# Kernel tuning notes

Hardware: AMD Instinct MI355X
Metric: run time of the kernel (lower is better)

## Reference

```python
import jax, jax.numpy as jnp
import numpy as np

B, T = 4, 512
IN, OUT, D, HID = 80, 4096, 512, 1024
E, NB, LPB = 4, 2, 4
NL = NB * LPB
H, M = 8, 64
LB, LA, SL, SR = 4, 1, 2, 1


def setup_inputs():
    key = jax.random.key(0)
    it = iter(jax.random.split(key, 40))
    def nrm(shape, s=0.02):
        return jax.random.normal(next(it), shape, jnp.float32) * s
    return {
        'x': jax.random.normal(next(it), (B, T, IN), jnp.float32),
        'seq_len': jax.random.randint(next(it), (B,), T // 2, T + 1),
        'emb_w1': nrm((IN, HID)), 'emb_b1': jnp.zeros((HID,), jnp.float32),
        'emb_w2': nrm((HID, D)), 'emb_wo': nrm((D, OUT)),
        'f0_w1': nrm((E, IN, HID)), 'f0_b1': jnp.zeros((E, HID), jnp.float32),
        'f0_w2': nrm((E, HID, D)), 'f0_router': nrm((D, E)),
        'f0_fb': nrm((LB, D), 0.1), 'f0_fa': nrm((LA, D), 0.1),
        'f_w1': nrm((NL - 1, E, D, HID)), 'f_b1': jnp.zeros((NL - 1, E, HID), jnp.float32),
        'f_w2': nrm((NL - 1, E, HID, D)), 'f_router': nrm((NL - 1, D, E)),
        'f_fb': nrm((NL - 1, LB, D), 0.1), 'f_fa': nrm((NL - 1, LA, D), 0.1),
        'attn_wq': nrm((NB, D, D)), 'attn_wk': nrm((NB, D, D)),
        'attn_wv': nrm((NB, D, D)), 'attn_wo': nrm((NB, D, D)),
        'attn_mk': nrm((NB, M, D)), 'attn_mv': nrm((NB, M, D)),
        'ln_g': jnp.ones((NB, D), jnp.float32), 'ln_b': jnp.zeros((NB, D), jnp.float32),
        'out_w': nrm((D, OUT)), 'out_b': jnp.zeros((OUT,), jnp.float32),
    }


def _fsmn_memory(p, fb, fa):
    # m[t] = p[t] + sum_k fb[k]*p[t-(k+1)*SL] + sum_j fa[j]*p[t+(j+1)*SR]  (depthwise)
    m = p
    for k in range(fb.shape[0]):
        off = (k + 1) * SL
        past = jnp.pad(p, ((0, 0), (off, 0), (0, 0)))[:, :p.shape[1]]
        m = m + past * fb[k]
    for j in range(fa.shape[0]):
        off = (j + 1) * SR
        fut = jnp.pad(p, ((0, 0), (0, off), (0, 0)))[:, off:]
        m = m + fut * fa[j]
    return m


def _pe(dtype):
    pos = jnp.arange(T, dtype=jnp.float32)[:, None]
    div = jnp.exp(jnp.arange(0, D, 2, dtype=jnp.float32) * (-np.log(10000.0) / D))
    pe = jnp.zeros((T, D), jnp.float32)
    pe = pe.at[:, 0::2].set(jnp.sin(pos * div)).at[:, 1::2].set(jnp.cos(pos * div))
    return pe.astype(dtype)


def _layernorm(x, g, b):
    mu = jnp.mean(x, -1, keepdims=True)
    var = jnp.var(x, -1, keepdims=True)
    return (x - mu) * jax.lax.rsqrt(var + 1e-5) * g + b


def reference(x, seq_len, emb_w1, emb_b1, emb_w2, emb_wo,
              f0_w1, f0_b1, f0_w2, f0_router, f0_fb, f0_fa,
              f_w1, f_b1, f_w2, f_router, f_fb, f_fa,
              attn_wq, attn_wk, attn_wv, attn_wo, attn_mk, attn_mv,
              ln_g, ln_b, out_w, out_b):
    tok_mask = jnp.arange(T)[None, :] < seq_len[:, None]  # [B,T] valid frames

    # embed sub-network (router features; detached as in Net.forward)
    embed = jax.nn.relu(x @ emb_w1 + emb_b1) @ emb_w2      # [B,T,D]
    embed_out = embed @ emb_wo                             # [B,T,OUT]
    embed_r = jax.lax.stop_gradient(embed)

    def moe_fsmn(xi, w1, b1, w2, router, fb, fa, skip):
        gates = jax.nn.softmax(embed_r @ router, axis=-1)  # [B,T,E]
        g = jnp.max(gates, axis=-1)
        disp = jax.nn.one_hot(jnp.argmax(gates, -1), E, dtype=xi.dtype) * g[..., None]
        h = jax.nn.relu(jnp.einsum('bti,eih->beth', xi, w1) + b1[None, :, None, :])
        p = jnp.einsum('beth,ehd->betd', h, w2)            # low-rank expert proj
        p = jnp.einsum('bte,betd->btd', disp, p)           # top-1 combine
        m = _fsmn_memory(p, fb, fa)
        if skip:
            m = m + xi
        imp = jnp.sum(gates * tok_mask[..., None].astype(gates.dtype), axis=(0, 1))
        aux = jnp.var(imp) / (jnp.mean(imp) ** 2 + 1e-9)   # importance cv^2
        return m, aux

    def attention(xi, wq, wk, wv, wo, mk, mv, g, b):
        dh = D // H
        q = (xi @ wq).reshape(B, T, H, dh)
        k = jnp.concatenate([xi @ wk, jnp.broadcast_to(mk, (B, M, D))], 1).reshape(B, T + M, H, dh)
        v = jnp.concatenate([xi @ wv, jnp.broadcast_to(mv, (B, M, D))], 1).reshape(B, T + M, H, dh)
        scores = jnp.einsum('bthd,bshd->bhts', q, k) / np.sqrt(dh).astype(np.float32)
        key_ok = jnp.concatenate([tok_mask, jnp.ones((B, M), bool)], 1)  # memory keys never masked
        scores = jnp.where(key_ok[:, None, None, :], scores, jnp.float32(-1e9))
        a = jax.nn.softmax(scores, -1)
        o = jnp.einsum('bhts,bshd->bthd', a, v).reshape(B, T, D) @ wo
        return _layernorm(xi + o, g, b)

    auxes = []
    cur = x
    li = 0
    for blk in range(NB):
        for _ in range(LPB):
            if li == 0:
                cur, aux = moe_fsmn(cur, f0_w1, f0_b1, f0_w2, f0_router, f0_fb, f0_fa, False)
            else:
                j = li - 1
                cur, aux = moe_fsmn(cur, f_w1[j], f_b1[j], f_w2[j], f_router[j], f_fb[j], f_fa[j], True)
            auxes.append(aux)
            li += 1
        if blk == 0:
            cur = cur + _pe(cur.dtype)[None]
        cur = attention(cur, attn_wq[blk], attn_wk[blk], attn_wv[blk], attn_wo[blk],
                        attn_mk[blk], attn_mv[blk], ln_g[blk], ln_b[blk])
    out = cur @ out_w + out_b
    return out, embed_out, jnp.stack(auxes).sum()
```

## Files before the change

### kernel.cpp

```cpp
#include <hip/hip_runtime.h>
#include <hip/hip_bf16.h>


typedef __bf16 bf16x8 __attribute__((ext_vector_type(8)));
typedef float f32x4 __attribute__((ext_vector_type(4)));

#define B_ 4
#define T_ 512
#define IN_ 80
#define OUT_ 4096
#define D_ 512
#define HID_ 1024
#define E_ 4
#define H_ 8
#define DH_ 64
#define M_ 64
#define BT_ (B_ * T_)
#define TKV_ (T_ + M_)
#define RBLK_ (BT_ / 4)

__device__ __forceinline__ unsigned pk2(float a, float b) {
    unsigned short ua = __builtin_bit_cast(unsigned short, (__bf16)a);
    unsigned short ub = __builtin_bit_cast(unsigned short, (__bf16)b);
    return (unsigned)ua | ((unsigned)ub << 16);
}
__device__ __forceinline__ unsigned pkh2(__bf16 a, __bf16 b) {
    unsigned short ua = __builtin_bit_cast(unsigned short, a);
    unsigned short ub = __builtin_bit_cast(unsigned short, b);
    return (unsigned)ua | ((unsigned)ub << 16);
}

__global__ __launch_bounds__(256) void gemm80_k(
    const float* __restrict__ A,
    const float* __restrict__ Bw,
    const float* __restrict__ bias,
    float* __restrict__ C)
{
    __shared__ float As[80][68];
    __shared__ float Bs[80][68];
    int m0 = blockIdx.y * 64, n0 = blockIdx.x * 64;
    int tid = threadIdx.x;
#pragma unroll
    for (int i = 0; i < 5; i++) {
        int idx = tid + 256 * i;
        int m = idx / 20, c = idx % 20;
        float4 f = *(const float4*)&A[(size_t)(m0 + m) * 80 + c * 4];
        As[c * 4 + 0][m] = f.x; As[c * 4 + 1][m] = f.y;
        As[c * 4 + 2][m] = f.z; As[c * 4 + 3][m] = f.w;
    }
#pragma unroll
    for (int i = 0; i < 5; i++) {
        int idx = tid + 256 * i;
        int k = idx / 16, c = idx % 16;
        float4 f = *(const float4*)&Bw[(size_t)k * 1024 + n0 + c * 4];
        *(float4*)&Bs[k][c * 4] = f;
    }
    __syncthreads();
    int tx = tid & 15, ty = tid >> 4;
    float acc[4][4];
#pragma unroll
    for (int j = 0; j < 4; j++)
#pragma unroll
        for (int i = 0; i < 4; i++) acc[j][i] = 0.f;
#pragma unroll 8
    for (int k = 0; k < 80; k++) {
        float4 a = *(const float4*)&As[k][ty * 4];
        float4 b = *(const float4*)&Bs[k][tx * 4];
        float av[4] = {a.x, a.y, a.z, a.w};
        float bv[4] = {b.x, b.y, b.z, b.w};
#pragma unroll
        for (int j = 0; j < 4; j++)
#pragma unroll
            for (int i = 0; i < 4; i++) acc[j][i] += av[j] * bv[i];
    }
#pragma unroll
    for (int j = 0; j < 4; j++) {
        size_t row = (size_t)(m0 + ty * 4 + j);
        float4 o;
        o.x = fmaxf(acc[j][0] + bias[n0 + tx * 4 + 0], 0.f);
        o.y = fmaxf(acc[j][1] + bias[n0 + tx * 4 + 1], 0.f);
        o.z = fmaxf(acc[j][2] + bias[n0 + tx * 4 + 2], 0.f);
        o.w = fmaxf(acc[j][3] + bias[n0 + tx * 4 + 3], 0.f);
        *(float4*)&C[row * 1024 + n0 + tx * 4] = o;
    }
}

__global__ void wr2_k(const float* __restrict__ w2,
                      const float* __restrict__ r0,
                      const float* __restrict__ rl,
                      float* __restrict__ R2)
{
    int wv = threadIdx.x >> 6, lane = threadIdx.x & 63;
    int h = blockIdx.x * 4 + wv;
    const float* wrow = w2 + (size_t)h * 512;
    float w[8];
#pragma unroll
    for (int i = 0; i < 8; i++) w[i] = wrow[lane + 64 * i];
    for (int l = 0; l < 8; l++) {
        const float* rp = (l == 0) ? r0 : rl + (size_t)(l - 1) * 2048;
        double a0 = 0, a1 = 0, a2 = 0, a3 = 0;
#pragma unroll
        for (int i = 0; i < 8; i++) {
            int d = lane + 64 * i;
            float4 r = *(const float4*)&rp[d * 4];
            a0 += (double)w[i] * (double)r.x;
            a1 += (double)w[i] * (double)r.y;
            a2 += (double)w[i] * (double)r.z;
            a3 += (double)w[i] * (double)r.w;
        }
        for (int off = 32; off; off >>= 1) {
            a0 += __shfl_xor(a0, off); a1 += __shfl_xor(a1, off);
            a2 += __shfl_xor(a2, off); a3 += __shfl_xor(a3, off);
        }
        if (lane == 0) {
            float4 o = make_float4((float)a0, (float)a1, (float)a2, (float)a3);
            *(float4*)&R2[((size_t)l * 1024 + h) * 4] = o;
        }
    }
}

__global__ __launch_bounds__(256) void routerall_k(
    const float* __restrict__ h,
    const float* __restrict__ R2,
    const int* __restrict__ seq_len,
    int* __restrict__ eid,
    float* __restrict__ gatev,
    float* __restrict__ impPart)
{
    __shared__ float impLoc[4][32];
    int wv = threadIdx.x >> 6, lane = threadIdx.x & 63;
    int tok = blockIdx.x * 4 + wv;
    const float* hr = h + (size_t)tok * 1024;
    float acc[8][4];
#pragma unroll
    for (int l = 0; l < 8; l++)
#pragma unroll
        for (int e = 0; e < 4; e++) acc[l][e] = 0.f;
    for (int i = 0; i < 16; i++) {
        int d = lane + 64 * i;
        float hv = hr[d];
#pragma unroll
        for (int l = 0; l < 8; l++) {
            float4 r = *(const float4*)&R2[((size_t)l * 1024 + d) * 4];
            acc[l][0] += hv * r.x; acc[l][1] += hv * r.y;
            acc[l][2] += hv * r.z; acc[l][3] += hv * r.w;
        }
    }
    for (int off = 32; off; off >>= 1) {
#pragma unroll
        for (int l = 0; l < 8; l++)
#pragma unroll
            for (int e = 0; e < 4; e++) acc[l][e] += __shfl_xor(acc[l][e], off);
    }
    if (lane == 0) {
        int b = tok >> 9, t = tok & 511;
        bool valid = t < seq_len[b];
        for (int l = 0; l < 8; l++) {
            float lg[4] = {acc[l][0], acc[l][1], acc[l][2], acc[l][3]};
            float mx = fmaxf(fmaxf(lg[0], lg[1]), fmaxf(lg[2], lg[3]));
            float g[4], s = 0.f;
            for (int e = 0; e < 4; e++) { g[e] = expf(lg[e] - mx); s += g[e]; }
            float inv = 1.f / s;
            int am = 0; float bv = g[0];
            for (int e = 1; e < 4; e++) if (g[e] > bv) { bv = g[e]; am = e; }
            eid[l * BT_ + tok] = am;
            gatev[l * BT_ + tok] = bv * inv;
            for (int e = 0; e < 4; e++)
                impLoc[wv][l * 4 + e] = valid ? g[e] * inv : 0.f;
        }
    }
    __syncthreads();
    int tid = threadIdx.x;
    if (tid < 32) {
        float s = impLoc[0][tid] + impLoc[1][tid] + impLoc[2][tid] + impLoc[3][tid];
        impPart[(size_t)blockIdx.x * 32 + tid] = s;
    }
}

__global__ void cvtw_k(const float* __restrict__ src, __bf16* __restrict__ dst,
                       int nsh, int kpsh, int Ksrc)
{
    int idx = blockIdx.x * 256 + threadIdx.x;
    int cprsh = nsh - 3;
    int row = idx >> cprsh;
    int chunk = idx & ((1 << cprsh) - 1);
    int e = row >> kpsh, k = row & ((1 << kpsh) - 1);
    int n = chunk * 8;
    uint4 pk;
    if (k < Ksrc) {
        const float* sp = src + (((size_t)e * Ksrc + k) << nsh) + n;
        float4 f0 = *(const float4*)sp;
        float4 f1 = *(const float4*)(sp + 4);
        pk = make_uint4(pk2(f0.x, f0.y), pk2(f0.z, f0.w),
                        pk2(f1.x, f1.y), pk2(f1.z, f1.w));
    } else pk = make_uint4(0, 0, 0, 0);
    *(uint4*)&dst[(((size_t)row) << nsh) + n] = pk;
}

__global__ void gathera_k(const float* __restrict__ src, int lda,
                          const int* __restrict__ sorted,
                          __bf16* __restrict__ dst, int kpsh, int Ksrc)
{
    int idx = blockIdx.x * 256 + threadIdx.x;
    int cprsh = kpsh - 3;
    int row = idx >> cprsh;
    int chunk = idx & ((1 << cprsh) - 1);
    int k0 = chunk * 8;
    uint4 pk;
    if (k0 < Ksrc) {
        const float* sp = src + (size_t)sorted[row] * lda + k0;
        float4 f0 = *(const float4*)sp;
        float4 f1 = *(const float4*)(sp + 4);
        pk = make_uint4(pk2(f0.x, f0.y), pk2(f0.z, f0.w),
                        pk2(f1.x, f1.y), pk2(f1.z, f1.w));
    } else pk = make_uint4(0, 0, 0, 0);
    *(uint4*)&dst[((size_t)row << kpsh) + k0] = pk;
}

template<bool W1OUT>
__global__ __launch_bounds__(256) void egemm_k(
    const __bf16* __restrict__ Ag, const __bf16* __restrict__ Bh,
    const float* __restrict__ bias,
    __bf16* __restrict__ Cb, float* __restrict__ Cf,
    int N, int Kpad,
    const int* __restrict__ seg, const int* __restrict__ sorted,
    const float* __restrict__ scale)
{
    __shared__ __align__(16) __bf16 As[2][128 * 64];
    __shared__ __align__(16) __bf16 Bs[2][64 * 64];

    int e = blockIdx.z;
    int row0 = seg[e], cnt = seg[e + 1] - row0;
    int m0 = blockIdx.y * 128;
    if (m0 >= cnt) return;
    int n0 = blockIdx.x * 64;
    const __bf16* Bp = Bh + (size_t)e * Kpad * N;

    int tid = threadIdx.x;
    int arow = tid >> 1, ahalf = tid & 1;
    const __bf16* aptr = Ag + (size_t)(row0 + m0 + arow) * Kpad + ahalf * 32;
    int asb = arow * 64;
    int ac0 = ahalf * 4;
    int arx = arow & 7;
    int bn = tid & 63, bkc = tid >> 6;
    const __bf16* bptr = Bp + n0 + bn;
    int bsb = bn * 64;
    int brx = bn & 7;

    int lane = tid & 63, wid = tid >> 6;
    int wm = wid & 1, wn = wid >> 1;
    int l15 = lane & 15, quad = lane >> 4;

    int aoff[4][2], boff[2][2];
#pragma unroll
    for (int mt = 0; mt < 4; mt++) {
        int m = wm * 64 + mt * 16 + l15;
#pragma unroll
        for (int s = 0; s < 2; s++)
            aoff[mt][s] = m * 64 + (((s * 4 + quad) ^ (m & 7)) * 8);
    }
#pragma unroll
    for (int nt = 0; nt < 2; nt++) {
        int n = wn * 32 + nt * 16 + l15;
#pragma unroll
        for (int s = 0; s < 2; s++)
            boff[nt][s] = n * 64 + (((s * 4 + quad) ^ (n & 7)) * 8);
    }

    f32x4 acc[4][2];
#pragma unroll
    for (int mt = 0; mt < 4; mt++)
#pragma unroll
        for (int nt = 0; nt < 2; nt++)
#pragma unroll
            for (int r = 0; r < 4; r++) acc[mt][nt][r] = 0.f;

    uint4 rA[4]; unsigned rB[8];
    auto stage = [&](int k0) {
#pragma unroll
        for (int j = 0; j < 4; j++) rA[j] = *(const uint4*)(aptr + k0 + j * 8);
#pragma unroll
        for (int c = 0; c < 2; c++) {
            int kk = k0 + (bkc * 2 + c) * 8;
#pragma unroll
            for (int i = 0; i < 4; i++)
                rB[c * 4 + i] = pkh2(bptr[(size_t)(kk + 2 * i) * N],
                                     bptr[(size_t)(kk + 2 * i + 1) * N]);
        }
    };
    auto commit = [&](int buf) {
#pragma unroll
        for (int j = 0; j < 4; j++)
            *(uint4*)&As[buf][asb + (((ac0 + j) ^ arx) * 8)] = rA[j];
#pragma unroll
        for (int c = 0; c < 2; c++)
            *(uint4*)&Bs[buf][bsb + (((bkc * 2 + c) ^ brx) * 8)] =
                make_uint4(rB[c * 4 + 0], rB[c * 4 + 1], rB[c * 4 + 2], rB[c * 4 + 3]);
    };

    stage(0); commit(0); __syncthreads();
    int nt_ = Kpad >> 6;
    for (int t = 0; t < nt_; t++) {
        int buf = t & 1;
        if (t + 1 < nt_) stage((t + 1) << 6);
        bf16x8 af[4][2], bfr[2][2];
#pragma unroll
        for (int mt = 0; mt < 4; mt++)
#pragma unroll
            for (int s = 0; s < 2; s++)
                af[mt][s] = *(const bf16x8*)&As[buf][aoff[mt][s]];
#pragma unroll
        for (int ntx = 0; ntx < 2; ntx++)
#pragma unroll
            for (int s = 0; s < 2; s++)
                bfr[ntx][s] = *(const bf16x8*)&Bs[buf][boff[ntx][s]];
#pragma unroll
        for (int mt = 0; mt < 4; mt++)
#pragma unroll
            for (int ntx = 0; ntx < 2; ntx++)
#pragma unroll
                for (int s = 0; s < 2; s++)
                    acc[mt][ntx] = __builtin_amdgcn_mfma_f32_16x16x32_bf16(
                        af[mt][s], bfr[ntx][s], acc[mt][ntx], 0, 0, 0);
        if (t + 1 < nt_) commit(buf ^ 1);
        __syncthreads();
    }

#pragma unroll
    for (int mt = 0; mt < 4; mt++) {
#pragma unroll
        for (int r = 0; r < 4; r++) {
            int m = m0 + wm * 64 + mt * 16 + quad * 4 + r;
            if (m >= cnt) continue;
            if (W1OUT) {
                size_t ci = (size_t)(row0 + m);
#pragma unroll
                for (int ntx = 0; ntx < 2; ntx++) {
                    int col = n0 + wn * 32 + ntx * 16 + l15;
                    float v = acc[mt][ntx][r] + bias[e * N + col];
                    Cb[ci * N + col] = (__bf16)fmaxf(v, 0.f);
                }
            } else {
                int tok = sorted[row0 + m];
                float sc = scale[tok];
#pragma unroll
                for (int ntx = 0; ntx < 2; ntx++) {
                    int col = n0 + wn * 32 + ntx * 16 + l15;
                    Cf[(size_t)tok * N + col] = acc[mt][ntx][r] * sc;
                }
            }
        }
    }
}

#define MBM 128
#define MBN 64
#define MBK 32
#define LDAS 40

template<bool RELU, bool BIAS>
__global__ __launch_bounds__(256) void mgemm_k(
    const float* __restrict__ A, int lda,
    const float* __restrict__ Bw, const float* __restrict__ bias,
    float* __restrict__ C, int ldc, int M, int N, int K, int remM)
{
    __shared__ __align__(16) __bf16 As[MBM * LDAS];
    __shared__ __align__(16) __bf16 Bs[MBN * LDAS];

    int m0 = blockIdx.y * MBM;
    int n0 = blockIdx.x * MBN;

    int tid = threadIdx.x;
    int arow = tid >> 1, ahalf = tid & 1;
    const float* aptr = A + (size_t)(m0 + arow) * lda + ahalf * 16;
    int asw = (arow >> 3) & 3;
    int bn = tid & 63, bkc = tid >> 6;
    int bcs = bkc ^ ((bn >> 3) & 3);

    int lane = tid & 63, wid = tid >> 6;
    int wm = wid & 1, wn = wid >> 1;
    int l15 = lane & 15, quad = lane >> 4;

    int aoff[4], boff[2];
#pragma unroll
    for (int mt = 0; mt < 4; mt++) {
        int m = wm * 64 + mt * 16 + l15;
        aoff[mt] = m * LDAS + (quad ^ ((m >> 3) & 3)) * 8;
    }
#pragma unroll
    for (int nt = 0; nt < 2; nt++) {
        int n = wn * 32 + nt * 16 + l15;
        boff[nt] = n * LDAS + (quad ^ ((n >> 3) & 3)) * 8;
    }

    f32x4 acc[4][2];
#pragma unroll
    for (int mt = 0; mt < 4; mt++)
#pragma unroll
        for (int nt = 0; nt < 2; nt++)
#pragma unroll
            for (int r = 0; r < 4; r++) acc[mt][nt][r] = 0.f;

    for (int k0 = 0; k0 < K; k0 += MBK) {
#pragma unroll
        for (int cc = 0; cc < 2; cc++) {
            float4 f0 = *(const float4*)(aptr + k0 + cc * 8);
            float4 f1 = *(const float4*)(aptr + k0 + cc * 8 + 4);
            uint4 pk = make_uint4(pk2(f0.x, f0.y), pk2(f0.z, f0.w),
                                  pk2(f1.x, f1.y), pk2(f1.z, f1.w));
            int cs = (ahalf * 2 + cc) ^ asw;
            *(uint4*)&As[arow * LDAS + cs * 8] = pk;
        }
        {
            float f[8];
            int kk = k0 + bkc * 8;
#pragma unroll
            for (int i = 0; i < 8; i++)
                f[i] = Bw[(size_t)(kk + i) * N + n0 + bn];
            uint4 pk = make_uint4(pk2(f[0], f[1]), pk2(f[2], f[3]),
                                  pk2(f[4], f[5]), pk2(f[6], f[7]));
            *(uint4*)&Bs[bn * LDAS + bcs * 8] = pk;
        }
        __syncthreads();
        bf16x8 af[4], bfm[2];
#pragma unroll
        for (int mt = 0; mt < 4; mt++) af[mt] = *(const bf16x8*)&As[aoff[mt]];
#pragma unroll
        for (int nt = 0; nt < 2; nt++) bfm[nt] = *(const bf16x8*)&Bs[boff[nt]];
#pragma unroll
        for (int mt = 0; mt < 4; mt++)
#pragma unroll
            for (int nt = 0; nt < 2; nt++)
                acc[mt][nt] = __builtin_amdgcn_mfma_f32_16x16x32_bf16(
                    af[mt], bfm[nt], acc[mt][nt], 0, 0, 0);
        __syncthreads();
    }

#pragma unroll
    for (int mt = 0; mt < 4; mt++) {
#pragma unroll
        for (int r = 0; r < 4; r++) {
            int mi = wm * 64 + mt * 16 + quad * 4 + r;
            int m = m0 + mi;
            size_t crow = (size_t)m;
            if (remM) crow = (size_t)m + (size_t)(m >> 9) * remM;
#pragma unroll
            for (int nt = 0; nt < 2; nt++) {
                int col = n0 + wn * 32 + nt * 16 + l15;
                float v = acc[mt][nt][r];
                if (BIAS) v += bias[col];
                if (RELU) v = fmaxf(v, 0.f);
                C[crow * (size_t)ldc + col] = v;
            }
        }
    }
}

__global__ __launch_bounds__(256) void qkv_k(
    const float* __restrict__ A,
    const float* __restrict__ wq, const float* __restrict__ wk,
    const float* __restrict__ wv,
    float* __restrict__ qo, float* __restrict__ ko, float* __restrict__ vo)
{
    __shared__ __align__(16) __bf16 As[MBM * LDAS];
    __shared__ __align__(16) __bf16 Bs[MBN * LDAS];

    int n0g = blockIdx.x * MBN;
    int which = n0g >> 9;
    int n0 = n0g & 511;
    const float* Bp = (which == 0) ? wq : (which == 1) ? wk : wv;
    float* Cp = (which == 0) ? qo : (which == 1) ? ko : vo;
    int m0 = blockIdx.y * MBM;

    int tid = threadIdx.x;
    int arow = tid >> 1, ahalf = tid & 1;
    const float* aptr = A + (size_t)(m0 + arow) * D_ + ahalf * 16;
    int asw = (arow >> 3) & 3;
    int bn = tid & 63, bkc = tid >> 6;
    int bcs = bkc ^ ((bn >> 3) & 3);

    int lane = tid & 63, wid = tid >> 6;
    int wm = wid & 1, wn = wid >> 1;
    int l15 = lane & 15, quad = lane >> 4;

    int aoff[4], boff[2];
#pragma unroll
    for (int mt = 0; mt < 4; mt++) {
        int m = wm * 64 + mt * 16 + l15;
        aoff[mt] = m * LDAS + (quad ^ ((m >> 3) & 3)) * 8;
    }
#pragma unroll
    for (int nt = 0; nt < 2; nt++) {
        int n = wn * 32 + nt * 16 + l15;
        boff[nt] = n * LDAS + (quad ^ ((n >> 3) & 3)) * 8;
    }

    f32x4 acc[4][2];
#pragma unroll
    for (int mt = 0; mt < 4; mt++)
#pragma unroll
        for (int nt = 0; nt < 2; nt++)
#pragma unroll
            for (int r = 0; r < 4; r++) acc[mt][nt][r] = 0.f;

    for (int k0 = 0; k0 < D_; k0 += MBK) {
#pragma unroll
        for (int cc = 0; cc < 2; cc++) {
            float4 f0 = *(const float4*)(aptr + k0 + cc * 8);
            float4 f1 = *(const float4*)(aptr + k0 + cc * 8 + 4);
            uint4 pk = make_uint4(pk2(f0.x, f0.y), pk2(f0.z, f0.w),
                                  pk2(f1.x, f1.y), pk2(f1.z, f1.w));
            int cs = (ahalf * 2 + cc) ^ asw;
            *(uint4*)&As[arow * LDAS + cs * 8] = pk;
        }
        {
            float f[8];
            int kk = k0 + bkc * 8;
#pragma unroll
            for (int i = 0; i < 8; i++)
                f[i] = Bp[(size_t)(kk + i) * D_ + n0 + bn];
            uint4 pk = make_uint4(pk2(f[0], f[1]), pk2(f[2], f[3]),
                                  pk2(f[4], f[5]), pk2(f[6], f[7]));
            *(uint4*)&Bs[bn * LDAS + bcs * 8] = pk;
        }
        __syncthreads();
        bf16x8 af[4], bfm[2];
#pragma unroll
        for (int mt = 0; mt < 4; mt++) af[mt] = *(const bf16x8*)&As[aoff[mt]];
#pragma unroll
        for (int nt = 0; nt < 2; nt++) bfm[nt] = *(const bf16x8*)&Bs[boff[nt]];
#pragma unroll
        for (int mt = 0; mt < 4; mt++)
#pragma unroll
            for (int nt = 0; nt < 2; nt++)
                acc[mt][nt] = __builtin_amdgcn_mfma_f32_16x16x32_bf16(
                    af[mt], bfm[nt], acc[mt][nt], 0, 0, 0);
        __syncthreads();
    }

#pragma unroll
    for (int mt = 0; mt < 4; mt++) {
#pragma unroll
        for (int r = 0; r < 4; r++) {
            int mi = wm * 64 + mt * 16 + quad * 4 + r;
            int m = m0 + mi;
            size_t crow = which ? (size_t)(m + (m >> 9) * M_) : (size_t)m;
#pragma unroll
            for (int nt = 0; nt < 2; nt++) {
                int col = n0 + wn * 32 + nt * 16 + l15;
                Cp[crow * (size_t)D_ + col] = acc[mt][nt][r];
            }
        }
    }
}

__global__ void bucketall_k(const int* __restrict__ eidA, int* __restrict__ sortedA,
                            int* __restrict__ segA)
{
    __shared__ int cnt[E_]; __shared__ int cur[E_];
    int l = blockIdx.x;
    const int* eid = eidA + l * BT_;
    int* sorted = sortedA + l * BT_;
    int* seg = segA + l * 8;
    int tid = threadIdx.x;
    if (tid < E_) cnt[tid] = 0;
    __syncthreads();
    for (int t = tid; t < BT_; t += 256) atomicAdd(&cnt[eid[t]], 1);
    __syncthreads();
    if (tid == 0) {
        int o = 0;
        for (int e = 0; e < E_; e++) { seg[e] = o; cur[e] = o; o += cnt[e]; }
        seg[E_] = o;
    }
    __syncthreads();
    for (int t = tid; t < BT_; t += 256) {
        int pos = atomicAdd(&cur[eid[t]], 1);
        sorted[pos] = t;
    }
}

__global__ void fsmn_k(const float* __restrict__ p, const float* __restrict__ fb,
                       const float* __restrict__ fa, float* __restrict__ cur, int skip)
{
    int idx = blockIdx.x * 256 + threadIdx.x;
    int d = idx & 511;
    int t = (idx >> 9) & 511;
    float m = p[idx];
#pragma unroll
    for (int k = 0; k < 4; k++) {
        int tt = t - 2 * (k + 1);
        if (tt >= 0) m += fb[k * D_ + d] * p[idx - D_ * 2 * (k + 1)];
    }
    if (t + 1 < T_) m += fa[d] * p[idx + D_];
    if (skip) m += cur[idx];
    cur[idx] = m;
}

__global__ void addpe_k(float* __restrict__ cur) {
    int idx = blockIdx.x * 256 + threadIdx.x;
    int d = idx & 511, t = (idx >> 9) & 511;
    float div = expf((float)(d & ~1) * (-9.210340371976184f / (float)D_));
    float ang = (float)t * div;
    cur[idx] += (d & 1) ? cosf(ang) : sinf(ang);
}

__global__ void fillmem_k(const float* __restrict__ mk, const float* __restrict__ mv,
                          float* __restrict__ kbuf, float* __restrict__ vbuf)
{
    int idx = blockIdx.x * 256 + threadIdx.x;
    int d = idx & 511, m = (idx >> 9) & 63, b = idx >> 15;
    size_t row = (size_t)b * TKV_ + T_ + m;
    kbuf[row * D_ + d] = mk[m * D_ + d];
    vbuf[row * D_ + d] = mv[m * D_ + d];
}

#define QR 16
__global__ __launch_bounds__(256) void attn_k(
    const float* __restrict__ q, const float* __restrict__ kbuf,
    const float* __restrict__ vbuf, const int* __restrict__ seq_len,
    float* __restrict__ attno)
{
    __shared__ float kv[64 * 69];
    __shared__ float qs[QR][64];
    __shared__ float sc[QR][TKV_];
    int b = blockIdx.z, h = blockIdx.y, t0 = blockIdx.x * QR;
    int tid = threadIdx.x, w = tid >> 6, lane = tid & 63;
    int r0 = w * 4;
#pragma unroll
    for (int i = 0; i < 4; i++) {
        int idx = tid + 256 * i;
        int r = idx >> 6, d = idx & 63;
        qs[r][d] = q[((size_t)(b * T_) + t0 + r) * D_ + h * DH_ + d] * 0.125f;
    }
    int sl = seq_len[b];
    for (int s0 = 0; s0 < TKV_; s0 += 64) {
        __syncthreads();
#pragma unroll
        for (int i = 0; i < 16; i++) {
            int idx = tid + 256 * i;
            int key = idx >> 6, d = idx & 63;
            kv[d * 69 + key] = kbuf[((size_t)b * TKV_ + s0 + key) * D_ + h * DH_ + d];
        }
        __syncthreads();
        float a0 = 0, a1 = 0, a2 = 0, a3 = 0;
#pragma unroll 4
        for (int d = 0; d < 64; d++) {
            float kvv = kv[d * 69 + lane];
            a0 += qs[r0 + 0][d] * kvv;
            a1 += qs[r0 + 1][d] * kvv;
            a2 += qs[r0 + 2][d] * kvv;
            a3 += qs[r0 + 3][d] * kvv;
        }
        int sa = s0 + lane;
        bool ok = (sa >= T_ || sa < sl);
        sc[r0 + 0][sa] = ok ? a0 : -1e9f;
        sc[r0 + 1][sa] = ok ? a1 : -1e9f;
        sc[r0 + 2][sa] = ok ? a2 : -1e9f;
        sc[r0 + 3][sa] = ok ? a3 : -1e9f;
    }
    float inv[4];
#pragma unroll
    for (int r = 0; r < 4; r++) {
        float mx = -1e30f;
        for (int s = lane; s < TKV_; s += 64) mx = fmaxf(mx, sc[r0 + r][s]);
        for (int off = 32; off; off >>= 1) mx = fmaxf(mx, __shfl_xor(mx, off));
        float sum = 0.f;
        for (int s = lane; s < TKV_; s += 64) {
            float e2 = expf(sc[r0 + r][s] - mx); sc[r0 + r][s] = e2; sum += e2;
        }
        for (int off = 32; off; off >>= 1) sum += __shfl_xor(sum, off);
        inv[r] = 1.f / sum;
    }
    float o0 = 0, o1 = 0, o2 = 0, o3 = 0;
    for (int s0 = 0; s0 < TKV_; s0 += 64) {
        __syncthreads();
#pragma unroll
        for (int i = 0; i < 16; i++) {
            int idx = tid + 256 * i;
            int key = idx >> 6, d = idx & 63;
            kv[key * 69 + d] = vbuf[((size_t)b * TKV_ + s0 + key) * D_ + h * DH_ + d];
        }
        __syncthreads();
#pragma unroll 4
        for (int j = 0; j < 64; j++) {
            float vv = kv[j * 69 + lane];
            o0 += sc[r0 + 0][s0 + j] * vv;
            o1 += sc[r0 + 1][s0 + j] * vv;
            o2 += sc[r0 + 2][s0 + j] * vv;
            o3 += sc[r0 + 3][s0 + j] * vv;
        }
    }
    size_t base = ((size_t)(b * T_) + t0 + r0) * D_ + h * DH_ + lane;
    attno[base + 0 * D_] = o0 * inv[0];
    attno[base + 1 * D_] = o1 * inv[1];
    attno[base + 2 * D_] = o2 * inv[2];
    attno[base + 3 * D_] = o3 * inv[3];
}

__global__ void ln_k(const float* __restrict__ o, const float* __restrict__ g,
                     const float* __restrict__ bb, float* __restrict__ cur)
{
    int w = threadIdx.x >> 6, lane = threadIdx.x & 63;
    size_t row = (size_t)(blockIdx.x * 4 + w);
    float v[8]; float s = 0.f;
#pragma unroll
    for (int i = 0; i < 8; i++) {
        int d = lane + 64 * i;
        v[i] = cur[row * D_ + d] + o[row * D_ + d];
        s += v[i];
    }
    for (int off = 32; off; off >>= 1) s += __shfl_xor(s, off);
    float mu = s * (1.f / D_);
    float vs = 0.f;
#pragma unroll
    for (int i = 0; i < 8; i++) { float dd = v[i] - mu; vs += dd * dd; }
    for (int off = 32; off; off >>= 1) vs += __shfl_xor(vs, off);
    float rstd = rsqrtf(vs * (1.f / D_) + 1e-5f);
#pragma unroll
    for (int i = 0; i < 8; i++) {
        int d = lane + 64 * i;
        cur[row * D_ + d] = (v[i] - mu) * rstd * g[d] + bb[d];
    }
}

__global__ __launch_bounds__(256) void aux_k(const float* __restrict__ impPart,
                                             float* __restrict__ outp)
{
    __shared__ float red[8][32];
    __shared__ float imp[32];
    int tid = threadIdx.x;
    int c = tid & 31, p = tid >> 5;
    float s = 0.f;
    for (int b = p; b < RBLK_; b += 8) s += impPart[(size_t)b * 32 + c];
    red[p][c] = s;
    __syncthreads();
    if (tid < 32) {
        float t = 0.f;
#pragma unroll
        for (int i = 0; i < 8; i++) t += red[i][tid];
        imp[tid] = t;
    }
    __syncthreads();
    if (tid == 0) {
        float total = 0.f;
        for (int l = 0; l < 8; l++) {
            const float* ip = imp + l * 4;
            float m = (ip[0] + ip[1] + ip[2] + ip[3]) * 0.25f;
            float var = 0.f;
            for (int e = 0; e < 4; e++) { float d = ip[e] - m; var += d * d; }
            var *= 0.25f;
            total += var / (m * m + 1e-9f);
        }
        *outp = total;
    }
}

extern "C" void kernel_launch(void* const* d_in, const int* in_sizes, int n_in,
                              void* d_out, int out_size, void* d_ws, size_t ws_size,
                              hipStream_t stream)
{
    (void)in_sizes; (void)n_in; (void)out_size; (void)ws_size;
    const float* x        = (const float*)d_in[0];
    const int*   seqlen   = (const int*)d_in[1];
    const float* emb_w1   = (const float*)d_in[2];
    const float* emb_b1   = (const float*)d_in[3];
    const float* emb_w2   = (const float*)d_in[4];
    const float* emb_wo   = (const float*)d_in[5];
    const float* f0_w1    = (const float*)d_in[6];
    const float* f0_b1    = (const float*)d_in[7];
    const float* f0_w2    = (const float*)d_in[8];
    const float* f0_router= (const float*)d_in[9];
    const float* f0_fb    = (const float*)d_in[10];
    const float* f0_fa    = (const float*)d_in[11];
    const float* f_w1     = (const float*)d_in[12];
    const float* f_b1     = (const float*)d_in[13];
    const float* f_w2     = (const float*)d_in[14];
    const float* f_router = (const float*)d_in[15];
    const float* f_fb     = (const float*)d_in[16];
    const float* f_fa     = (const float*)d_in[17];
    const float* attn_wq  = (const float*)d_in[18];
    const float* attn_wk  = (const float*)d_in[19];
    const float* attn_wv  = (const float*)d_in[20];
    const float* attn_wo  = (const float*)d_in[21];
    const float* attn_mk  = (const float*)d_in[22];
    const float* attn_mv  = (const float*)d_in[23];
    const float* ln_g     = (const float*)d_in[24];
    const float* ln_b     = (const float*)d_in[25];
    const float* out_w    = (const float*)d_in[26];
    const float* out_b    = (const float*)d_in[27];

    float* out0 = (float*)d_out;
    float* out1 = out0 + (size_t)BT_ * OUT_;
    float* out2 = out1 + (size_t)BT_ * OUT_;

    float* fws = (float*)d_ws;
    size_t o = 0;
    float* embedF = fws + o; o += (size_t)BT_ * D_;
    float* curB   = fws + o; o += (size_t)BT_ * D_;
    float* hbuf   = fws + o; o += (size_t)BT_ * HID_;
    float* pbuf   = fws + o; o += (size_t)BT_ * D_;
    float* kbuf   = fws + o; o += (size_t)B_ * TKV_ * D_;
    float* vbuf   = fws + o; o += (size_t)B_ * TKV_ * D_;
    float* gatev  = fws + o; o += (size_t)8 * BT_;
    float* impPart= fws + o; o += (size_t)RBLK_ * 32;
    float* R2     = fws + o; o += (size_t)8 * 1024 * 4;
    int* eid     = (int*)(fws + o); o += (size_t)8 * BT_;
    int* sortedA = (int*)(fws + o); o += (size_t)8 * BT_;
    int* segA    = (int*)(fws + o); o += 64;
    __bf16* Ag    = (__bf16*)hbuf;
    __bf16* hbufh = (__bf16*)(hbuf + (size_t)BT_ * D_ / 2);
    __bf16* w1h   = (__bf16*)kbuf;
    __bf16* w2h   = (__bf16*)vbuf;
    float* qbuf  = pbuf;
    float* attno = hbuf;
    float* tmpo  = hbuf + (size_t)BT_ * D_;

    gemm80_k<<<dim3(HID_ / 64, BT_ / 64, 1), 256, 0, stream>>>(x, emb_w1, emb_b1, hbuf);
    wr2_k<<<256, 256, 0, stream>>>(emb_w2, f0_router, f_router, R2);
    routerall_k<<<RBLK_, 256, 0, stream>>>(hbuf, R2, seqlen, eid, gatev, impPart);
    bucketall_k<<<8, 256, 0, stream>>>(eid, sortedA, segA);
    mgemm_k<false,false><<<dim3(D_/MBN, BT_/MBM, 1), 256, 0, stream>>>(
        hbuf, HID_, emb_w2, nullptr, embedF, D_, BT_, D_, HID_, 0);
    mgemm_k<false,false><<<dim3(OUT_/MBN, BT_/MBM, 1), 256, 0, stream>>>(
        embedF, D_, emb_wo, nullptr, out1, OUT_, BT_, OUT_, D_, 0);

    for (int l = 0; l < 8; l++) {
        const float* w1  = (l == 0) ? f0_w1 : f_w1 + (size_t)(l-1) * E_ * D_ * HID_;
        const float* b1p = (l == 0) ? f0_b1 : f_b1 + (size_t)(l-1) * E_ * HID_;
        const float* w2  = (l == 0) ? f0_w2 : f_w2 + (size_t)(l-1) * E_ * HID_ * D_;
        const float* fbp = (l == 0) ? f0_fb : f_fb + (size_t)(l-1) * 4 * D_;
        const float* fap = (l == 0) ? f0_fa : f_fa + (size_t)(l-1) * 1 * D_;
        const float* Ain = (l == 0) ? x : curB;
        int lda  = (l == 0) ? IN_ : D_;
        int Ks   = (l == 0) ? IN_ : D_;
        int Kp   = (l == 0) ? 128 : 512;
        int kpsh = (l == 0) ? 7 : 9;
        const int* seg = segA + l * 8;
        const int* sorted = sortedA + l * BT_;

        cvtw_k<<<E_ * Kp * HID_ / 8 / 256, 256, 0, stream>>>(w1, w1h, 10, kpsh, Ks);
        cvtw_k<<<E_ * HID_ * D_ / 8 / 256, 256, 0, stream>>>(w2, w2h, 9, 10, HID_);
        gathera_k<<<BT_ * Kp / 8 / 256, 256, 0, stream>>>(Ain, lda, sorted, Ag, kpsh, Ks);

        egemm_k<true><<<dim3(HID_/64, BT_/128, E_), 256, 0, stream>>>(
            Ag, w1h, b1p, hbufh, nullptr, HID_, Kp, seg, nullptr, nullptr);
        egemm_k<false><<<dim3(D_/64, BT_/128, E_), 256, 0, stream>>>(
            hbufh, w2h, nullptr, nullptr, pbuf, D_, HID_, seg, sorted, gatev + l * BT_);
        fsmn_k<<<BT_*D_/256, 256, 0, stream>>>(pbuf, fbp, fap, curB, (l > 0) ? 1 : 0);

        if (l == 3) addpe_k<<<BT_*D_/256, 256, 0, stream>>>(curB);

        if (l == 3 || l == 7) {
            int ab = (l == 3) ? 0 : 1;
            const float* wq = attn_wq + (size_t)ab * D_ * D_;
            const float* wk = attn_wk + (size_t)ab * D_ * D_;
            const float* wv = attn_wv + (size_t)ab * D_ * D_;
            const float* wo = attn_wo + (size_t)ab * D_ * D_;
            const float* mk = attn_mk + (size_t)ab * M_ * D_;
            const float* mv = attn_mv + (size_t)ab * M_ * D_;
            const float* g  = ln_g + (size_t)ab * D_;
            const float* bb = ln_b + (size_t)ab * D_;

            qkv_k<<<dim3(3 * D_ / MBN, BT_ / MBM, 1), 256, 0, stream>>>(
                curB, wq, wk, wv, qbuf, kbuf, vbuf);
            fillmem_k<<<B_*M_*D_/256, 256, 0, stream>>>(mk, mv, kbuf, vbuf);
            attn_k<<<dim3(T_/QR, H_, B_), 256, 0, stream>>>(qbuf, kbuf, vbuf, seqlen, attno);
            mgemm_k<false,false><<<dim3(D_/MBN, BT_/MBM, 1), 256, 0, stream>>>(
                attno, D_, wo, nullptr, tmpo, D_, BT_, D_, D_, 0);
            ln_k<<<BT_/4, 256, 0, stream>>>(tmpo, g, bb, curB);
        }
    }

    mgemm_k<false,true><<<dim3(OUT_/MBN, BT_/MBM, 1), 256, 0, stream>>>(
        curB, D_, out_w, out_b, out0, OUT_, BT_, OUT_, D_, 0);
    aux_k<<<1, 256, 0, stream>>>(impPart, out2);
}
```

Measured before the change: 1.423 ms.

## Double-buffer dense GEMMs with bf16 weights and skip masked attention key tiles

Replaces the generic dense GEMM with a double-buffered kernel using K-tiles of 64. Weights are converted to bf16 up front, so the B operand is read at half width and global loads overlap the MFMA work. The attention kernel now visits only key tiles up to the sequence length plus the memory tile, and vectorises its score and PV inner loops. It adds extra conversion launches per call and reuses scratch buffers for the bf16 weights, which risks aliasing if those buffers are still live.

```diff
diff --git a/kernel.cpp b/kernel.cpp
--- a/kernel.cpp
+++ b/kernel.cpp
@@ -353,26 +353,150 @@
     }
 }
 
+template<bool BIAS>
+__global__ __launch_bounds__(256) void dgemm_k(
+    const float* __restrict__ A,
+    const __bf16* __restrict__ Bh,
+    const float* __restrict__ bias,
+    float* __restrict__ C,
+    int N, int K)
+{
+    __shared__ __align__(16) __bf16 As[2][128 * 64];
+    __shared__ __align__(16) __bf16 Bs[2][64 * 64];
+
+    int m0 = blockIdx.y * 128, n0 = blockIdx.x * 64;
+    int tid = threadIdx.x;
+    int arow = tid >> 1, ahalf = tid & 1;
+    const float* aptr = A + (size_t)(m0 + arow) * K + ahalf * 32;
+    int asb = arow * 64, ac0 = ahalf * 4, arx = arow & 7;
+    int bn = tid & 63, bkc = tid >> 6;
+    const __bf16* bptr = Bh + n0 + bn;
+    int bsb = bn * 64, brx = bn & 7;
+
+    int lane = tid & 63, wid = tid >> 6;
+    int wm = wid & 1, wn = wid >> 1;
+    int l15 = lane & 15, quad = lane >> 4;
+
+    int aoff[4][2], boff[2][2];
+#pragma unroll
+    for (int mt = 0; mt < 4; mt++) {
+        int m = wm * 64 + mt * 16 + l15;
+#pragma unroll
+        for (int s = 0; s < 2; s++)
+            aoff[mt][s] = m * 64 + (((s * 4 + quad) ^ (m & 7)) * 8);
+    }
+#pragma unroll
+    for (int nt = 0; nt < 2; nt++) {
+        int n = wn * 32 + nt * 16 + l15;
+#pragma unroll
+        for (int s = 0; s < 2; s++)
+            boff[nt][s] = n * 64 + (((s * 4 + quad) ^ (n & 7)) * 8);
+    }
+
+    f32x4 acc[4][2];
+#pragma unroll
+    for (int mt = 0; mt < 4; mt++)
+#pragma unroll
+        for (int nt = 0; nt < 2; nt++)
+#pragma unroll
+            for (int r = 0; r < 4; r++) acc[mt][nt][r] = 0.f;
+
+    uint4 rA[4]; unsigned rB[8];
+    auto stage = [&](int k0) {
+#pragma unroll
+        for (int j = 0; j < 4; j++) {
+            float4 f0 = *(const float4*)(aptr + k0 + j * 8);
+            float4 f1 = *(const float4*)(aptr + k0 + j * 8 + 4);
+            rA[j] = make_uint4(pk2(f0.x, f0.y), pk2(f0.z, f0.w),
+                               pk2(f1.x, f1.y), pk2(f1.z, f1.w));
+        }
+#pragma unroll
+        for (int c = 0; c < 2; c++) {
+            int kk = k0 + (bkc * 2 + c) * 8;
+#pragma unroll
+            for (int i = 0; i < 4; i++)
+                rB[c * 4 + i] = pkh2(bptr[(size_t)(kk + 2 * i) * N],
+                                     bptr[(size_t)(kk + 2 * i + 1) * N]);
+        }
+    };
+    auto commit = [&](int buf) {
+#pragma unroll
+        for (int j = 0; j < 4; j++)
+            *(uint4*)&As[buf][asb + (((ac0 + j) ^ arx) * 8)] = rA[j];
+#pragma unroll
+        for (int c = 0; c < 2; c++)
+            *(uint4*)&Bs[buf][bsb + (((bkc * 2 + c) ^ brx) * 8)] =
+                make_uint4(rB[c * 4 + 0], rB[c * 4 + 1], rB[c * 4 + 2], rB[c * 4 + 3]);
+    };
+
+    stage(0); commit(0); __syncthreads();
+    int nt_ = K >> 6;
+    for (int t = 0; t < nt_; t++) {
+        int buf = t & 1;
+        if (t + 1 < nt_) stage((t + 1) << 6);
+        bf16x8 af[4][2], bfr[2][2];
+#pragma unroll
+        for (int mt = 0; mt < 4; mt++)
+#pragma unroll
+            for (int s = 0; s < 2; s++)
+                af[mt][s] = *(const bf16x8*)&As[buf][aoff[mt][s]];
+#pragma unroll
+        for (int ntx = 0; ntx < 2; ntx++)
+#pragma unroll
+            for (int s = 0; s < 2; s++)
+                bfr[ntx][s] = *(const bf16x8*)&Bs[buf][boff[ntx][s]];
+#pragma unroll
+        for (int mt = 0; mt < 4; mt++)
+#pragma unroll
+            for (int ntx = 0; ntx < 2; ntx++)
+#pragma unroll
+                for (int s = 0; s < 2; s++)
+                    acc[mt][ntx] = __builtin_amdgcn_mfma_f32_16x16x32_bf16(
+                        af[mt][s], bfr[ntx][s], acc[mt][ntx], 0, 0, 0);
+        if (t + 1 < nt_) commit(buf ^ 1);
+        __syncthreads();
+    }
+
+#pragma unroll
+    for (int mt = 0; mt < 4; mt++) {
+#pragma unroll
+        for (int r = 0; r < 4; r++) {
+            int m = m0 + wm * 64 + mt * 16 + quad * 4 + r;
+#pragma unroll
+            for (int ntx = 0; ntx < 2; ntx++) {
+                int col = n0 + wn * 32 + ntx * 16 + l15;
+                float v = acc[mt][ntx][r];
+                if (BIAS) v += bias[col];
+                C[(size_t)m * N + col] = v;
+            }
+        }
+    }
+}
+
 #define MBM 128
 #define MBN 64
 #define MBK 32
 #define LDAS 40
 
-template<bool RELU, bool BIAS>
-__global__ __launch_bounds__(256) void mgemm_k(
-    const float* __restrict__ A, int lda,
-    const float* __restrict__ Bw, const float* __restrict__ bias,
-    float* __restrict__ C, int ldc, int M, int N, int K, int remM)
+__global__ __launch_bounds__(256) void qkv_k(
+    const float* __restrict__ A,
+    const __bf16* __restrict__ wq, const __bf16* __restrict__ wk,
+    const __bf16* __restrict__ wv,
+    float* __restrict__ qo, float* __restrict__ ko, float* __restrict__ vo)
 {
     __shared__ __align__(16) __bf16 As[MBM * LDAS];
     __shared__ __align__(16) __bf16 Bs[MBN * LDAS];
 
+    int n0g = blockIdx.x * MBN;
+    int which = n0g >> 9;
+    int n0 = n0g & 511;
+    const __bf16* Bp = (which == 0) ? wq : (which == 1) ? wk : wv;
+    float* Cp = (which == 0) ? qo : (which == 1) ? ko : vo;
     int m0 = blockIdx.y * MBM;
-    int n0 = blockIdx.x * MBN;
 
     int tid = threadIdx.x;
     int arow = tid >> 1, ahalf = tid & 1;
-    const float* aptr = A + (size_t)(m0 + arow) * lda + ahalf * 16;
+    const float* aptr = A + (size_t)(m0 + arow) * D_ + ahalf * 16;
     int asw = (arow >> 3) & 3;
     int bn = tid & 63, bkc = tid >> 6;
     int bcs = bkc ^ ((bn >> 3) & 3);
@@ -401,7 +525,7 @@
 #pragma unroll
             for (int r = 0; r < 4; r++) acc[mt][nt][r] = 0.f;
 
-    for (int k0 = 0; k0 < K; k0 += MBK) {
+    for (int k0 = 0; k0 < D_; k0 += MBK) {
 #pragma unroll
         for (int cc = 0; cc < 2; cc++) {
             float4 f0 = *(const float4*)(aptr + k0 + cc * 8);
@@ -412,115 +536,13 @@
             *(uint4*)&As[arow * LDAS + cs * 8] = pk;
         }
         {
-            float f[8];
-            int kk = k0 + bkc * 8;
-#pragma unroll
-            for (int i = 0; i < 8; i++)
-                f[i] = Bw[(size_t)(kk + i) * N + n0 + bn];
-            uint4 pk = make_uint4(pk2(f[0], f[1]), pk2(f[2], f[3]),
-                                  pk2(f[4], f[5]), pk2(f[6], f[7]));
-            *(uint4*)&Bs[bn * LDAS + bcs * 8] = pk;
-        }
-        __syncthreads();
-        bf16x8 af[4], bfm[2];
-#pragma unroll
-        for (int mt = 0; mt < 4; mt++) af[mt] = *(const bf16x8*)&As[aoff[mt]];
-#pragma unroll
-        for (int nt = 0; nt < 2; nt++) bfm[nt] = *(const bf16x8*)&Bs[boff[nt]];
-#pragma unroll
-        for (int mt = 0; mt < 4; mt++)
-#pragma unroll
-            for (int nt = 0; nt < 2; nt++)
-                acc[mt][nt] = __builtin_amdgcn_mfma_f32_16x16x32_bf16(
-                    af[mt], bfm[nt], acc[mt][nt], 0, 0, 0);
-        __syncthreads();
-    }
-
-#pragma unroll
-    for (int mt = 0; mt < 4; mt++) {
-#pragma unroll
-        for (int r = 0; r < 4; r++) {
-            int mi = wm * 64 + mt * 16 + quad * 4 + r;
-            int m = m0 + mi;
-            size_t crow = (size_t)m;
-            if (remM) crow = (size_t)m + (size_t)(m >> 9) * remM;
-#pragma unroll
-            for (int nt = 0; nt < 2; nt++) {
-                int col = n0 + wn * 32 + nt * 16 + l15;
-                float v = acc[mt][nt][r];
-                if (BIAS) v += bias[col];
-                if (RELU) v = fmaxf(v, 0.f);
-                C[crow * (size_t)ldc + col] = v;
-            }
-        }
-    }
-}
-
-__global__ __launch_bounds__(256) void qkv_k(
-    const float* __restrict__ A,
-    const float* __restrict__ wq, const float* __restrict__ wk,
-    const float* __restrict__ wv,
-    float* __restrict__ qo, float* __restrict__ ko, float* __restrict__ vo)
-{
-    __shared__ __align__(16) __bf16 As[MBM * LDAS];
-    __shared__ __align__(16) __bf16 Bs[MBN * LDAS];
-
-    int n0g = blockIdx.x * MBN;
-    int which = n0g >> 9;
-    int n0 = n0g & 511;
-    const float* Bp = (which == 0) ? wq : (which == 1) ? wk : wv;
-    float* Cp = (which == 0) ? qo : (which == 1) ? ko : vo;
-    int m0 = blockIdx.y * MBM;
-
-    int tid = threadIdx.x;
-    int arow = tid >> 1, ahalf = tid & 1;
-    const float* aptr = A + (size_t)(m0 + arow) * D_ + ahalf * 16;
-    int asw = (arow >> 3) & 3;
-    int bn = tid & 63, bkc = tid >> 6;
-    int bcs = bkc ^ ((bn >> 3) & 3);
-
-    int lane = tid & 63, wid = tid >> 6;
-    int wm = wid & 1, wn = wid >> 1;
-    int l15 = lane & 15, quad = lane >> 4;
-
-    int aoff[4], boff[2];
-#pragma unroll
-    for (int mt = 0; mt < 4; mt++) {
-        int m = wm * 64 + mt * 16 + l15;
-        aoff[mt] = m * LDAS + (quad ^ ((m >> 3) & 3)) * 8;
-    }
-#pragma unroll
-    for (int nt = 0; nt < 2; nt++) {
-        int n = wn * 32 + nt * 16 + l15;
-        boff[nt] = n * LDAS + (quad ^ ((n >> 3) & 3)) * 8;
-    }
-
-    f32x4 acc[4][2];
-#pragma unroll
-    for (int mt = 0; mt < 4; mt++)
-#pragma unroll
-        for (int nt = 0; nt < 2; nt++)
-#pragma unroll
-            for (int r = 0; r < 4; r++) acc[mt][nt][r] = 0.f;
-
-    for (int k0 = 0; k0 < D_; k0 += MBK) {
-#pragma unroll
-        for (int cc = 0; cc < 2; cc++) {
-            float4 f0 = *(const float4*)(aptr + k0 + cc * 8);
-            float4 f1 = *(const float4*)(aptr + k0 + cc * 8 + 4);
-            uint4 pk = make_uint4(pk2(f0.x, f0.y), pk2(f0.z, f0.w),
-                                  pk2(f1.x, f1.y), pk2(f1.z, f1.w));
-            int cs = (ahalf * 2 + cc) ^ asw;
-            *(uint4*)&As[arow * LDAS + cs * 8] = pk;
-        }
-        {
-            float f[8];
+            __bf16 f[8];
             int kk = k0 + bkc * 8;
 #pragma unroll
             for (int i = 0; i < 8; i++)
                 f[i] = Bp[(size_t)(kk + i) * D_ + n0 + bn];
-            uint4 pk = make_uint4(pk2(f[0], f[1]), pk2(f[2], f[3]),
-                                  pk2(f[4], f[5]), pk2(f[6], f[7]));
+            uint4 pk = make_uint4(pkh2(f[0], f[1]), pkh2(f[2], f[3]),
+                                  pkh2(f[4], f[5]), pkh2(f[6], f[7]));
             *(uint4*)&Bs[bn * LDAS + bcs * 8] = pk;
         }
         __syncthreads();
@@ -620,9 +642,9 @@
     const float* __restrict__ vbuf, const int* __restrict__ seq_len,
     float* __restrict__ attno)
 {
-    __shared__ float kv[64 * 69];
-    __shared__ float qs[QR][64];
-    __shared__ float sc[QR][TKV_];
+    __shared__ float kv[64 * 68];
+    __shared__ float qs[QR][68];
+    __shared__ float sc[QR][584];
     int b = blockIdx.z, h = blockIdx.y, t0 = blockIdx.x * QR;
     int tid = threadIdx.x, w = tid >> 6, lane = tid & 63;
     int r0 = w * 4;
@@ -633,61 +655,92 @@
         qs[r][d] = q[((size_t)(b * T_) + t0 + r) * D_ + h * DH_ + d] * 0.125f;
     }
     int sl = seq_len[b];
-    for (int s0 = 0; s0 < TKV_; s0 += 64) {
+    int ntv = (sl + 63) >> 6;
+    int kg = lane & 15, quad = lane >> 4;
+    int myrow = r0 + quad;
+
+    for (int ti = 0; ti <= ntv; ti++) {
+        int t = (ti < ntv) ? ti : 8;
+        int s0 = t * 64;
+        __syncthreads();
+        {
+            const float* kp = kbuf + ((size_t)b * TKV_ + s0 + w * 16) * D_ + h * DH_ + lane;
+#pragma unroll
+            for (int jj = 0; jj < 4; jj++) {
+                float4 kf;
+                kf.x = kp[(jj * 4 + 0) * D_];
+                kf.y = kp[(jj * 4 + 1) * D_];
+                kf.z = kp[(jj * 4 + 2) * D_];
+                kf.w = kp[(jj * 4 + 3) * D_];
+                *(float4*)&kv[lane * 68 + w * 16 + jj * 4] = kf;
+            }
+        }
+        __syncthreads();
+        float a0 = 0, a1 = 0, a2 = 0, a3 = 0;
+#pragma unroll 8
+        for (int d = 0; d < 64; d++) {
+            float4 kf = *(const float4*)&kv[d * 68 + kg * 4];
+            float qv = qs[myrow][d];
+            a0 = fmaf(qv, kf.x, a0);
+            a1 = fmaf(qv, kf.y, a1);
+            a2 = fmaf(qv, kf.z, a2);
+            a3 = fmaf(qv, kf.w, a3);
+        }
+        int sb = s0 + kg * 4;
+        float4 o;
+        o.x = (sb + 0 >= T_ || sb + 0 < sl) ? a0 : -1e9f;
+        o.y = (sb + 1 >= T_ || sb + 1 < sl) ? a1 : -1e9f;
+        o.z = (sb + 2 >= T_ || sb + 2 < sl) ? a2 : -1e9f;
+        o.w = (sb + 3 >= T_ || sb + 3 < sl) ? a3 : -1e9f;
+        *(float4*)&sc[myrow][s0 + kg * 4] = o;
+    }
+    __syncthreads();
+
+    float inv[4];
+#pragma unroll
+    for (int r = 0; r < 4; r++) {
+        float mx = -1e30f;
+        for (int ti = 0; ti <= ntv; ti++) {
+            int s0 = ((ti < ntv) ? ti : 8) * 64;
+            mx = fmaxf(mx, sc[r0 + r][s0 + lane]);
+        }
+        for (int off = 32; off; off >>= 1) mx = fmaxf(mx, __shfl_xor(mx, off));
+        float sum = 0.f;
+        for (int ti = 0; ti <= ntv; ti++) {
+            int s0 = ((ti < ntv) ? ti : 8) * 64;
+            float e2 = expf(sc[r0 + r][s0 + lane] - mx);
+            sc[r0 + r][s0 + lane] = e2; sum += e2;
+        }
+        for (int off = 32; off; off >>= 1) sum += __shfl_xor(sum, off);
+        inv[r] = 1.f / sum;
+    }
+
+    float o0 = 0, o1 = 0, o2 = 0, o3 = 0;
+    for (int ti = 0; ti <= ntv; ti++) {
+        int t = (ti < ntv) ? ti : 8;
+        int s0 = t * 64;
         __syncthreads();
 #pragma unroll
         for (int i = 0; i < 16; i++) {
             int idx = tid + 256 * i;
             int key = idx >> 6, d = idx & 63;
-            kv[d * 69 + key] = kbuf[((size_t)b * TKV_ + s0 + key) * D_ + h * DH_ + d];
-        }
-        __syncthreads();
-        float a0 = 0, a1 = 0, a2 = 0, a3 = 0;
-#pragma unroll 4
-        for (int d = 0; d < 64; d++) {
-            float kvv = kv[d * 69 + lane];
-            a0 += qs[r0 + 0][d] * kvv;
-            a1 += qs[r0 + 1][d] * kvv;
-            a2 += qs[r0 + 2][d] * kvv;
-            a3 += qs[r0 + 3][d] * kvv;
-        }
-        int sa = s0 + lane;
-        bool ok = (sa >= T_ || sa < sl);
-        sc[r0 + 0][sa] = ok ? a0 : -1e9f;
-        sc[r0 + 1][sa] = ok ? a1 : -1e9f;
-        sc[r0 + 2][sa] = ok ? a2 : -1e9f;
-        sc[r0 + 3][sa] = ok ? a3 : -1e9f;
-    }
-    float inv[4];
-#pragma unroll
-    for (int r = 0; r < 4; r++) {
-        float mx = -1e30f;
-        for (int s = lane; s < TKV_; s += 64) mx = fmaxf(mx, sc[r0 + r][s]);
-        for (int off = 32; off; off >>= 1) mx = fmaxf(mx, __shfl_xor(mx, off));
-        float sum = 0.f;
-        for (int s = lane; s < TKV_; s += 64) {
-            float e2 = expf(sc[r0 + r][s] - mx); sc[r0 + r][s] = e2; sum += e2;
-        }
-        for (int off = 32; off; off >>= 1) sum += __shfl_xor(sum, off);
-        inv[r] = 1.f / sum;
-    }
-    float o0 = 0, o1 = 0, o2 = 0, o3 = 0;
-    for (int s0 = 0; s0 < TKV_; s0 += 64) {
-        __syncthreads();
-#pragma unroll
-        for (int i = 0; i < 16; i++) {
-            int idx = tid + 256 * i;
-            int key = idx >> 6, d = idx & 63;
-            kv[key * 69 + d] = vbuf[((size_t)b * TKV_ + s0 + key) * D_ + h * DH_ + d];
+            kv[key * 68 + d] = vbuf[((size_t)b * TKV_ + s0 + key) * D_ + h * DH_ + d];
         }
         __syncthreads();
 #pragma unroll 4
-        for (int j = 0; j < 64; j++) {
-            float vv = kv[j * 69 + lane];
-            o0 += sc[r0 + 0][s0 + j] * vv;
-            o1 += sc[r0 + 1][s0 + j] * vv;
-            o2 += sc[r0 + 2][s0 + j] * vv;
-            o3 += sc[r0 + 3][s0 + j] * vv;
+        for (int g = 0; g < 16; g++) {
+            float4 p0 = *(const float4*)&sc[r0 + 0][s0 + g * 4];
+            float4 p1 = *(const float4*)&sc[r0 + 1][s0 + g * 4];
+            float4 p2 = *(const float4*)&sc[r0 + 2][s0 + g * 4];
+            float4 p3 = *(const float4*)&sc[r0 + 3][s0 + g * 4];
+            float v0 = kv[(g * 4 + 0) * 68 + lane];
+            float v1 = kv[(g * 4 + 1) * 68 + lane];
+            float v2 = kv[(g * 4 + 2) * 68 + lane];
+            float v3 = kv[(g * 4 + 3) * 68 + lane];
+            o0 += p0.x * v0 + p0.y * v1 + p0.z * v2 + p0.w * v3;
+            o1 += p1.x * v0 + p1.y * v1 + p1.z * v2 + p1.w * v3;
+            o2 += p2.x * v0 + p2.y * v1 + p2.z * v2 + p2.w * v3;
+            o3 += p3.x * v0 + p3.y * v1 + p3.z * v2 + p3.w * v3;
         }
     }
     size_t base = ((size_t)(b * T_) + t0 + r0) * D_ + h * DH_ + lane;
@@ -811,6 +864,13 @@
     __bf16* hbufh = (__bf16*)(hbuf + (size_t)BT_ * D_ / 2);
     __bf16* w1h   = (__bf16*)kbuf;
     __bf16* w2h   = (__bf16*)vbuf;
+    __bf16* w2e_h = (__bf16*)vbuf;
+    __bf16* woe_h = (__bf16*)kbuf;
+    __bf16* outw_h= (__bf16*)kbuf;
+    __bf16* wqh   = (__bf16*)embedF;
+    __bf16* wkh   = wqh + (size_t)D_ * D_;
+    __bf16* wvh   = wkh + (size_t)D_ * D_;
+    __bf16* woh   = wvh + (size_t)D_ * D_;
     float* qbuf  = pbuf;
     float* attno = hbuf;
     float* tmpo  = hbuf + (size_t)BT_ * D_;
@@ -819,10 +879,12 @@
     wr2_k<<<256, 256, 0, stream>>>(emb_w2, f0_router, f_router, R2);
     routerall_k<<<RBLK_, 256, 0, stream>>>(hbuf, R2, seqlen, eid, gatev, impPart);
     bucketall_k<<<8, 256, 0, stream>>>(eid, sortedA, segA);
-    mgemm_k<false,false><<<dim3(D_/MBN, BT_/MBM, 1), 256, 0, stream>>>(
-        hbuf, HID_, emb_w2, nullptr, embedF, D_, BT_, D_, HID_, 0);
-    mgemm_k<false,false><<<dim3(OUT_/MBN, BT_/MBM, 1), 256, 0, stream>>>(
-        embedF, D_, emb_wo, nullptr, out1, OUT_, BT_, OUT_, D_, 0);
+    cvtw_k<<<256, 256, 0, stream>>>(emb_w2, w2e_h, 9, 10, HID_);
+    cvtw_k<<<1024, 256, 0, stream>>>(emb_wo, woe_h, 12, 9, D_);
+    dgemm_k<false><<<dim3(D_ / 64, BT_ / 128, 1), 256, 0, stream>>>(
+        hbuf, w2e_h, nullptr, embedF, D_, HID_);
+    dgemm_k<false><<<dim3(OUT_ / 64, BT_ / 128, 1), 256, 0, stream>>>(
+        embedF, woe_h, nullptr, out1, OUT_, D_);
 
     for (int l = 0; l < 8; l++) {
         const float* w1  = (l == 0) ? f0_w1 : f_w1 + (size_t)(l-1) * E_ * D_ * HID_;
@@ -861,17 +923,22 @@
             const float* g  = ln_g + (size_t)ab * D_;
             const float* bb = ln_b + (size_t)ab * D_;
 
+            cvtw_k<<<128, 256, 0, stream>>>(wq, wqh, 9, 9, D_);
+            cvtw_k<<<128, 256, 0, stream>>>(wk, wkh, 9, 9, D_);
+            cvtw_k<<<128, 256, 0, stream>>>(wv, wvh, 9, 9, D_);
+            cvtw_k<<<128, 256, 0, stream>>>(wo, woh, 9, 9, D_);
             qkv_k<<<dim3(3 * D_ / MBN, BT_ / MBM, 1), 256, 0, stream>>>(
-                curB, wq, wk, wv, qbuf, kbuf, vbuf);
+                curB, wqh, wkh, wvh, qbuf, kbuf, vbuf);
             fillmem_k<<<B_*M_*D_/256, 256, 0, stream>>>(mk, mv, kbuf, vbuf);
             attn_k<<<dim3(T_/QR, H_, B_), 256, 0, stream>>>(qbuf, kbuf, vbuf, seqlen, attno);
-            mgemm_k<false,false><<<dim3(D_/MBN, BT_/MBM, 1), 256, 0, stream>>>(
-                attno, D_, wo, nullptr, tmpo, D_, BT_, D_, D_, 0);
+            dgemm_k<false><<<dim3(D_ / 64, BT_ / 128, 1), 256, 0, stream>>>(
+                attno, woh, nullptr, tmpo, D_, D_);
             ln_k<<<BT_/4, 256, 0, stream>>>(tmpo, g, bb, curB);
         }
     }
 
-    mgemm_k<false,true><<<dim3(OUT_/MBN, BT_/MBM, 1), 256, 0, stream>>>(
-        curB, D_, out_w, out_b, out0, OUT_, BT_, OUT_, D_, 0);
+    cvtw_k<<<1024, 256, 0, stream>>>(out_w, outw_h, 12, 9, D_);
+    dgemm_k<true><<<dim3(OUT_ / 64, BT_ / 128, 1), 256, 0, stream>>>(
+        curB, outw_h, out_b, out0, OUT_, D_);
     aux_k<<<1, 256, 0, stream>>>(impPart, out2);
 }
```

Result: no change. 1.424 ms (+0.1%).
